# Optimization experiments

Hardware: AMD Instinct MI355X
Metric: run time of the kernel (lower is better)

The kernel has to match this reference:

```python
import jax, jax.numpy as jnp
import numpy as np

N_NODES = 50000
N_EDGES = 800000
D = 64  # all feature sizes


def setup_inputs() -> dict:
    key = jax.random.key(0)
    ks = jax.random.split(key, 16)

    def unif(k, shape, fan_out):
        stdv = 0.2 / np.sqrt(fan_out)
        return jax.random.uniform(k, shape, jnp.float32, -stdv, stdv)

    return {
        "Skipnode_in_feats": jax.random.normal(ks[0], (N_NODES, D), jnp.float32),
        "node_in_feats": jax.random.normal(ks[1], (N_NODES, D), jnp.float32),
        "edge_in_feats": jax.random.normal(ks[2], (N_EDGES, D), jnp.float32),
        "src": jax.random.randint(ks[3], (N_EDGES,), 0, N_NODES, jnp.int32),
        "dst": jax.random.randint(ks[4], (N_EDGES,), 0, N_NODES, jnp.int32),
        "weight_n2n_u": unif(ks[5], (D, D), D),
        "weight_n2n_v": unif(ks[6], (3 * D, D), D),
        "weight_e2n": unif(ks[7], (D, D), D),
        "bias_n": unif(ks[8], (D,), D),
        "weight_n2e_u": unif(ks[9], (D, D), D),
        "weight_n2e_v": unif(ks[10], (2 * D, D), D),
        "weight_e2e": unif(ks[11], (2 * D, D), D),
        "bias_e": unif(ks[12], (D,), D),
    }


def reference(Skipnode_in_feats, node_in_feats, edge_in_feats, src, dst,
              weight_n2n_u, weight_n2n_v, weight_e2n, bias_n,
              weight_n2e_u, weight_n2e_v, weight_e2e, bias_e):
    n_nodes = node_in_feats.shape[0]

    # node -> node messages: m_e = (X W_u)[src] + (E W_e2n)[e], mean over dst
    h1 = node_in_feats @ weight_n2n_u            # [N, D]
    e1 = edge_in_feats @ weight_e2n              # [E, D]
    m = h1[src] + e1                             # [E, D]
    summed = jax.ops.segment_sum(m, dst, num_segments=n_nodes)          # [N, D]
    deg = jax.ops.segment_sum(jnp.ones_like(dst, jnp.float32), dst,
                              num_segments=n_nodes)                     # [N]
    h_neigh = summed / jnp.maximum(deg, 1.0)[:, None]  # DGL mean: 0 for isolated

    h_total = jnp.concatenate([Skipnode_in_feats, node_in_feats, h_neigh], axis=1)
    h_out = h_total @ weight_n2n_v + bias_n      # [N, D]

    # edge update: e2 = (X W_n2e_u)[src] + ([S,X] W_n2e_v)[dst]
    hu = node_in_feats @ weight_n2e_u            # [N, D]
    hc = jnp.concatenate([Skipnode_in_feats, node_in_feats], axis=1)
    hv = hc @ weight_n2e_v                       # [N, D]
    e2 = hu[src] + hv[dst]                       # [E, D]
    e_total = jnp.concatenate([edge_in_feats, e2], axis=1)
    e_out = e_total @ weight_e2e + bias_e        # [E, D]

    return (h_out, e_out)
```

## Files before the change

### kernel.cpp

```cpp
#include <hip/hip_runtime.h>

#define N_NODES 50000
#define N_EDGES 800000
#define D 64
#define ET_PAD 68
#define NB 196

__global__ void fold_weights(const float* __restrict__ w_n2n_u,
                             const float* __restrict__ w_n2n_v,
                             const float* __restrict__ w_e2n,
                             const float* __restrict__ w_n2e_u,
                             const float* __restrict__ w_n2e_v,
                             float* __restrict__ w_e2e_dummy,
                             const float* __restrict__ w_e2e,
                             float* __restrict__ Wbig, float* __restrict__ WD) {
    int bidx = blockIdx.x;
    int j = threadIdx.x;
    const float* Ebot = w_e2e + 64 * 64;
    const float* Wv3  = w_n2n_v + 128 * 64;
    if (bidx < 512) {
        int k = bidx >> 2, q = bidx & 3;
        float v = 0.f;
        if (q == 0) {
            v = w_n2n_v[k * 64 + j];
        } else if (q == 1) {
            if (k >= 64) for (int t = 0; t < 64; ++t) v = fmaf(w_n2e_u[(k - 64) * 64 + t], Ebot[t * 64 + j], v);
        } else if (q == 2) {
            for (int t = 0; t < 64; ++t) v = fmaf(w_n2e_v[k * 64 + t], Ebot[t * 64 + j], v);
        } else {
            if (k >= 64) for (int t = 0; t < 64; ++t) v = fmaf(w_n2n_u[(k - 64) * 64 + t], Wv3[t * 64 + j], v);
        }
        Wbig[(size_t)k * 256 + q * 64 + j] = v;
    } else {
        int k = bidx - 512;
        float v = 0.f;
        for (int t = 0; t < 64; ++t) v = fmaf(w_e2n[k * 64 + t], Wv3[t * 64 + j], v);
        WD[k * 64 + j] = v;
    }
}

__global__ __launch_bounds__(256) void node_pre(
    const float* __restrict__ S, const float* __restrict__ X,
    const float* __restrict__ Wbig, const float* __restrict__ bias_n,
    float* __restrict__ h_out, float* __restrict__ AX, float* __restrict__ bvec) {
    __shared__ __align__(16) float inT[64 * ET_PAD];
    __shared__ __align__(16) float Wl[64 * 64];
    const int t = threadIdx.x;
    const int m0 = blockIdx.x * 64, q = blockIdx.y, c0 = q * 64;
    const int tx = t & 15, ty = t >> 4;
    float acc[4][4] = {{0.f}};
    for (int h = 0; h < 2; ++h) {
        const float* P = h ? X : S;
        #pragma unroll
        for (int i = 0; i < 16; ++i) {
            int idx = i * 256 + t;
            int ml = idx >> 6, kl = idx & 63;
            int m = m0 + ml;
            inT[kl * ET_PAD + ml] = (m < N_NODES) ? P[(size_t)m * 64 + kl] : 0.f;
        }
        #pragma unroll
        for (int i = 0; i < 16; ++i) {
            int idx = i * 256 + t;
            int kl = idx >> 6, jl = idx & 63;
            Wl[kl * 64 + jl] = Wbig[(size_t)(h * 64 + kl) * 256 + c0 + jl];
        }
        __syncthreads();
        #pragma unroll 4
        for (int kl = 0; kl < 64; ++kl) {
            float4 av = *(const float4*)&inT[kl * ET_PAD + ty * 4];
            float4 wv = *(const float4*)&Wl[kl * 64 + tx * 4];
            float a4[4] = {av.x, av.y, av.z, av.w};
            float w4[4] = {wv.x, wv.y, wv.z, wv.w};
            #pragma unroll
            for (int im = 0; im < 4; ++im)
                #pragma unroll
                for (int ij = 0; ij < 4; ++ij)
                    acc[im][ij] = fmaf(a4[im], w4[ij], acc[im][ij]);
        }
        __syncthreads();
    }
    #pragma unroll
    for (int im = 0; im < 4; ++im) {
        int m = m0 + ty * 4 + im;
        if (m >= N_NODES) continue;
        #pragma unroll
        for (int ij = 0; ij < 4; ++ij) {
            int jl = tx * 4 + ij;
            float v = acc[im][ij];
            if (q == 0)      h_out[(size_t)m * 64 + jl] = v + bias_n[jl];
            else if (q == 1) AX[(size_t)m * 128 + 2 * jl] = v;
            else if (q == 2) bvec[(size_t)m * 64 + jl] = v;
            else             AX[(size_t)m * 128 + 2 * jl + 1] = v;
        }
    }
}

__global__ void hist_k(const int* __restrict__ dst, int* __restrict__ counts) {
    int e = blockIdx.x * 256 + threadIdx.x;
    if (e < N_EDGES) atomicAdd(&counts[dst[e]], 1);
}

__global__ void scan1(const int* __restrict__ counts, int* __restrict__ bsum) {
    __shared__ int s[256];
    int t = threadIdx.x;
    int i = blockIdx.x * 256 + t;
    s[t] = (i < N_NODES) ? counts[i] : 0;
    __syncthreads();
    for (int off = 128; off > 0; off >>= 1) {
        if (t < off) s[t] += s[t + off];
        __syncthreads();
    }
    if (t == 0) bsum[blockIdx.x] = s[0];
}

__global__ void scan2(const int* __restrict__ bsum, int* __restrict__ boff) {
    __shared__ int s[256];
    int t = threadIdx.x;
    int v0 = (t < NB) ? bsum[t] : 0;
    s[t] = v0;
    __syncthreads();
    for (int off = 1; off < 256; off <<= 1) {
        int v = (t >= off) ? s[t - off] : 0;
        __syncthreads();
        s[t] += v;
        __syncthreads();
    }
    if (t < NB) boff[t] = s[t] - v0;
}

__global__ void scan3(const int* __restrict__ counts, const int* __restrict__ boff,
                      int* __restrict__ offsets, int* __restrict__ cursor) {
    __shared__ int s[256];
    int t = threadIdx.x;
    int i = blockIdx.x * 256 + t;
    int v0 = (i < N_NODES) ? counts[i] : 0;
    s[t] = v0;
    __syncthreads();
    for (int off = 1; off < 256; off <<= 1) {
        int v = (t >= off) ? s[t - off] : 0;
        __syncthreads();
        s[t] += v;
        __syncthreads();
    }
    int excl = s[t] - v0 + boff[blockIdx.x];
    if (i < N_NODES) { offsets[i] = excl; cursor[i] = excl; }
    if (i == N_NODES - 1) offsets[N_NODES] = excl + v0;
}

__global__ void scatter_k(const int* __restrict__ src, const int* __restrict__ dst,
                          int* __restrict__ cursor, int* __restrict__ perm,
                          int* __restrict__ sSrc, int* __restrict__ sDst) {
    int e = blockIdx.x * 256 + threadIdx.x;
    if (e < N_EDGES) {
        int d = dst[e];
        int p = atomicAdd(&cursor[d], 1);
        perm[p] = e;
        sSrc[p] = src[e];
        sDst[p] = d;
    }
}

__global__ __launch_bounds__(256) void edge_kernel(
    const float* __restrict__ E, const int* __restrict__ perm,
    const int* __restrict__ sSrc, const int* __restrict__ sDst,
    const float* __restrict__ W1g ,
    const float* __restrict__ WDg,
    const float* __restrict__ AX, const float* __restrict__ bvec,
    const float* __restrict__ bias_e,
    float* __restrict__ e_out, float* __restrict__ hpre) {
    __shared__ int sPerm[64];
    __shared__ int sDstL[64];
    __shared__ __align__(16) float sEt[64 * ET_PAD];

    const int t = threadIdx.x;
    const int p0 = blockIdx.x * 64;
    if (t < 64) {
        sPerm[t] = perm[p0 + t];
        sDstL[t] = sDst[p0 + t];
    }
    __syncthreads();

    const int j = t & 63;
    const int g = t >> 6;

    float acc1[16], acc2[16];
    const float bj = bias_e[j];
    #pragma unroll
    for (int r = 0; r < 16; ++r) {
        int pos = g * 16 + r;
        int is = sSrc[p0 + pos];
        int id = sDstL[pos];
        float2 ax = *(const float2*)&AX[(size_t)is * 128 + 2 * j];
        acc1[r] = bj + ax.x + bvec[(size_t)id * 64 + j];
        acc2[r] = ax.y;
    }

    #pragma unroll
    for (int i = 0; i < 16; ++i) {
        int idx = i * 256 + t;
        int r = idx >> 6, k = idx & 63;
        sEt[k * ET_PAD + r] = E[(size_t)sPerm[r] * 64 + k];
    }
    __syncthreads();

    #pragma unroll 4
    for (int k = 0; k < 64; ++k) {
        float w1 = W1g[k * 64 + j];
        float wd = WDg[k * 64 + j];
        const float4* ep = (const float4*)&sEt[k * ET_PAD + g * 16];
        #pragma unroll
        for (int q = 0; q < 4; ++q) {
            float4 ev = ep[q];
            acc1[4 * q + 0] = fmaf(ev.x, w1, acc1[4 * q + 0]);
            acc2[4 * q + 0] = fmaf(ev.x, wd, acc2[4 * q + 0]);
            acc1[4 * q + 1] = fmaf(ev.y, w1, acc1[4 * q + 1]);
            acc2[4 * q + 1] = fmaf(ev.y, wd, acc2[4 * q + 1]);
            acc1[4 * q + 2] = fmaf(ev.z, w1, acc1[4 * q + 2]);
            acc2[4 * q + 2] = fmaf(ev.z, wd, acc2[4 * q + 2]);
            acc1[4 * q + 3] = fmaf(ev.w, w1, acc1[4 * q + 3]);
            acc2[4 * q + 3] = fmaf(ev.w, wd, acc2[4 * q + 3]);
        }
    }

    #pragma unroll
    for (int r = 0; r < 16; ++r) {
        int e = sPerm[g * 16 + r];
        e_out[(size_t)e * 64 + j] = acc1[r];
    }

    int cur = sDstL[g * 16];
    float run = acc2[0];
    #pragma unroll
    for (int r = 1; r < 16; ++r) {
        int d = sDstL[g * 16 + r];
        if (d == cur) {
            run += acc2[r];
        } else {
            atomicAdd(&hpre[(size_t)cur * 64 + j], run);
            cur = d;
            run = acc2[r];
        }
    }
    atomicAdd(&hpre[(size_t)cur * 64 + j], run);
}

__global__ void node_final(float* __restrict__ h_out,
                           const float* __restrict__ hpre,
                           const int* __restrict__ offsets) {
    int i = blockIdx.x * blockDim.x + threadIdx.x;
    if (i < N_NODES * 64) {
        int n = i >> 6;
        float deg = (float)(offsets[n + 1] - offsets[n]);
        float r = 1.0f / fmaxf(deg, 1.0f);
        h_out[i] += hpre[i] * r;
    }
}

extern "C" void kernel_launch(void* const* d_in, const int* in_sizes, int n_in,
                              void* d_out, int out_size, void* d_ws, size_t ws_size,
                              hipStream_t stream) {
    const float* S       = (const float*)d_in[0];
    const float* X       = (const float*)d_in[1];
    const float* E       = (const float*)d_in[2];
    const int*   src     = (const int*)  d_in[3];
    const int*   dst     = (const int*)  d_in[4];
    const float* w_n2n_u = (const float*)d_in[5];
    const float* w_n2n_v = (const float*)d_in[6];
    const float* w_e2n   = (const float*)d_in[7];
    const float* bias_n  = (const float*)d_in[8];
    const float* w_n2e_u = (const float*)d_in[9];
    const float* w_n2e_v = (const float*)d_in[10];
    const float* w_e2e   = (const float*)d_in[11];
    const float* bias_e  = (const float*)d_in[12];

    const size_t ND = (size_t)N_NODES * 64;

    float* ws        = (float*)d_ws;
    float* hpre      = ws;
    int*   counts    = (int*)(ws + ND);
    int*   offsets   = counts + N_NODES;
    int*   cursor    = offsets + N_NODES + 1;
    int*   bsum      = cursor + N_NODES;
    int*   boff      = bsum + 200;
    int*   perm      = boff + 200;
    int*   sSrc      = perm + N_EDGES;
    int*   sDst      = sSrc + N_EDGES;
    float* AX        = (float*)(sDst + N_EDGES);
    float* bvec      = AX + (size_t)N_NODES * 128;
    float* Wbig      = bvec + ND;
    float* WD        = Wbig + 128 * 256;

    float* h_out = (float*)d_out;
    float* e_out = h_out + ND;

    hipMemsetAsync(hpre, 0, (ND + N_NODES) * sizeof(float), stream);

    fold_weights<<<576, 64, 0, stream>>>(w_n2n_u, w_n2n_v, w_e2n, w_n2e_u,
                                         w_n2e_v, nullptr, w_e2e, Wbig, WD);

    dim3 npGrid((N_NODES + 63) / 64, 4);
    node_pre<<<npGrid, 256, 0, stream>>>(S, X, Wbig, bias_n, h_out, AX, bvec);

    hist_k <<<(N_EDGES + 255) / 256, 256, 0, stream>>>(dst, counts);
    scan1  <<<NB, 256, 0, stream>>>(counts, bsum);
    scan2  <<<1, 256, 0, stream>>>(bsum, boff);
    scan3  <<<NB, 256, 0, stream>>>(counts, boff, offsets, cursor);
    scatter_k<<<(N_EDGES + 255) / 256, 256, 0, stream>>>(src, dst, cursor, perm, sSrc, sDst);

    edge_kernel<<<N_EDGES / 64, 256, 0, stream>>>(
        E, perm, sSrc, sDst, w_e2e, WD, AX, bvec, bias_e, e_out, hpre);

    node_final<<<(N_NODES * 64 + 255) / 256, 256, 0, stream>>>(h_out, hpre, offsets);
}
```

Measured before the change: 743.7 us.

## Use bf16 MFMA for edge GEMM and pack sorted edge records

Moves the per-edge 64x128 projection from scalar FMAs on an fp32 LDS tile to bf16 MFMA 16x16x32. Edge features and the concatenated weight matrix (w_e2e top plus folded WD) are converted to bf16. The scatter now writes packed int4 records (perm, src, dst) instead of three separate arrays, and each wave handles its own 16 edges without block-wide syncs. The goal is to cut ALU time and index-load traffic, at the cost of bf16 rounding error on the E-dependent terms.

```diff
diff --git a/kernel.cpp b/kernel.cpp
--- a/kernel.cpp
+++ b/kernel.cpp
@@ -6,14 +6,23 @@
 #define ET_PAD 68
 #define NB 196
 
+typedef __attribute__((ext_vector_type(8))) short short8;
+typedef __attribute__((ext_vector_type(4))) float f32x4;
+
+__device__ inline unsigned short f2bf(float f) {
+    unsigned u = __float_as_uint(f);
+    unsigned r = (u + 0x7FFFu + ((u >> 16) & 1u)) >> 16;
+    return (unsigned short)r;
+}
+
 __global__ void fold_weights(const float* __restrict__ w_n2n_u,
                              const float* __restrict__ w_n2n_v,
                              const float* __restrict__ w_e2n,
                              const float* __restrict__ w_n2e_u,
                              const float* __restrict__ w_n2e_v,
-                             float* __restrict__ w_e2e_dummy,
                              const float* __restrict__ w_e2e,
-                             float* __restrict__ Wbig, float* __restrict__ WD) {
+                             float* __restrict__ Wbig,
+                             unsigned short* __restrict__ WTbf) {
     int bidx = blockIdx.x;
     int j = threadIdx.x;
     const float* Ebot = w_e2e + 64 * 64;
@@ -31,11 +40,14 @@
             if (k >= 64) for (int t = 0; t < 64; ++t) v = fmaf(w_n2n_u[(k - 64) * 64 + t], Wv3[t * 64 + j], v);
         }
         Wbig[(size_t)k * 256 + q * 64 + j] = v;
-    } else {
+    } else if (bidx < 576) {
         int k = bidx - 512;
         float v = 0.f;
         for (int t = 0; t < 64; ++t) v = fmaf(w_e2n[k * 64 + t], Wv3[t * 64 + j], v);
-        WD[k * 64 + j] = v;
+        WTbf[(64 + j) * 64 + k] = f2bf(v);
+    } else {
+        int k = bidx - 576;
+        WTbf[j * 64 + k] = f2bf(w_e2e[k * 64 + j]);
     }
 }
 
@@ -148,96 +160,89 @@
 }
 
 __global__ void scatter_k(const int* __restrict__ src, const int* __restrict__ dst,
-                          int* __restrict__ cursor, int* __restrict__ perm,
-                          int* __restrict__ sSrc, int* __restrict__ sDst) {
+                          int* __restrict__ cursor, int4* __restrict__ sEdge) {
     int e = blockIdx.x * 256 + threadIdx.x;
     if (e < N_EDGES) {
         int d = dst[e];
         int p = atomicAdd(&cursor[d], 1);
-        perm[p] = e;
-        sSrc[p] = src[e];
-        sDst[p] = d;
+        sEdge[p] = make_int4(e, src[e], d, 0);
     }
 }
 
 __global__ __launch_bounds__(256) void edge_kernel(
-    const float* __restrict__ E, const int* __restrict__ perm,
-    const int* __restrict__ sSrc, const int* __restrict__ sDst,
-    const float* __restrict__ W1g ,
-    const float* __restrict__ WDg,
+    const float* __restrict__ E, const int4* __restrict__ sEdge,
+    const unsigned short* __restrict__ WTbf,
     const float* __restrict__ AX, const float* __restrict__ bvec,
     const float* __restrict__ bias_e,
     float* __restrict__ e_out, float* __restrict__ hpre) {
-    __shared__ int sPerm[64];
-    __shared__ int sDstL[64];
-    __shared__ __align__(16) float sEt[64 * ET_PAD];
+    __shared__ __align__(16) unsigned short sEt[64 * 64];
+    __shared__ __align__(16) float sOut[64 * 128];
 
     const int t = threadIdx.x;
+    const int lane = t & 63;
+    const int w = t >> 6;
     const int p0 = blockIdx.x * 64;
-    if (t < 64) {
-        sPerm[t] = perm[p0 + t];
-        sDstL[t] = sDst[p0 + t];
-    }
-    __syncthreads();
-
-    const int j = t & 63;
-    const int g = t >> 6;
-
-    float acc1[16], acc2[16];
+    const int l15 = lane & 15, qd = lane >> 4;
+    const int j = lane;
+
+    float2 axv[16];
+    float  bv[16];
+    int    permv[16], dstv[16];
+    #pragma unroll
+    for (int r = 0; r < 16; ++r) {
+        int4 ed = sEdge[p0 + 16 * w + r];
+        permv[r] = ed.x;
+        dstv[r]  = ed.z;
+        axv[r] = *(const float2*)&AX[(size_t)ed.y * 128 + 2 * j];
+        bv[r]  = bvec[(size_t)ed.z * 64 + j];
+    }
+
+    #pragma unroll
+    for (int i = 0; i < 8; ++i) {
+        int idx = i * 64 + lane;
+        int r  = idx >> 5;
+        int kp = idx & 31;
+        int pe = sEdge[p0 + 16 * w + r].x;
+        float2 ev = *(const float2*)&E[(size_t)pe * 64 + 2 * kp];
+        unsigned pk = ((unsigned)f2bf(ev.y) << 16) | (unsigned)f2bf(ev.x);
+        *(unsigned*)&sEt[(16 * w + r) * 64 + 2 * kp] = pk;
+    }
+
+    const short8 a0 = *(const short8*)&sEt[(16 * w + l15) * 64 +  0 + qd * 8];
+    const short8 a1 = *(const short8*)&sEt[(16 * w + l15) * 64 + 32 + qd * 8];
+    #pragma unroll
+    for (int tt = 0; tt < 8; ++tt) {
+        const short8 b0 = *(const short8*)&WTbf[(16 * tt + l15) * 64 +  0 + qd * 8];
+        const short8 b1 = *(const short8*)&WTbf[(16 * tt + l15) * 64 + 32 + qd * 8];
+        f32x4 d = {0.f, 0.f, 0.f, 0.f};
+        d = __builtin_amdgcn_mfma_f32_16x16x32_bf16(a0, b0, d, 0, 0, 0);
+        d = __builtin_amdgcn_mfma_f32_16x16x32_bf16(a1, b1, d, 0, 0, 0);
+        int colw = (tt < 4) ? (16 * tt + l15) : (16 * (tt - 4) + l15);
+        int pos  = (tt < 4) ? (2 * colw) : (2 * colw + 1);
+        #pragma unroll
+        for (int reg = 0; reg < 4; ++reg)
+            sOut[(16 * w + qd * 4 + reg) * 128 + pos] = d[reg];
+    }
+
     const float bj = bias_e[j];
+    float acc2[16];
     #pragma unroll
     for (int r = 0; r < 16; ++r) {
-        int pos = g * 16 + r;
-        int is = sSrc[p0 + pos];
-        int id = sDstL[pos];
-        float2 ax = *(const float2*)&AX[(size_t)is * 128 + 2 * j];
-        acc1[r] = bj + ax.x + bvec[(size_t)id * 64 + j];
-        acc2[r] = ax.y;
-    }
-
-    #pragma unroll
-    for (int i = 0; i < 16; ++i) {
-        int idx = i * 256 + t;
-        int r = idx >> 6, k = idx & 63;
-        sEt[k * ET_PAD + r] = E[(size_t)sPerm[r] * 64 + k];
-    }
-    __syncthreads();
-
-    #pragma unroll 4
-    for (int k = 0; k < 64; ++k) {
-        float w1 = W1g[k * 64 + j];
-        float wd = WDg[k * 64 + j];
-        const float4* ep = (const float4*)&sEt[k * ET_PAD + g * 16];
-        #pragma unroll
-        for (int q = 0; q < 4; ++q) {
-            float4 ev = ep[q];
-            acc1[4 * q + 0] = fmaf(ev.x, w1, acc1[4 * q + 0]);
-            acc2[4 * q + 0] = fmaf(ev.x, wd, acc2[4 * q + 0]);
-            acc1[4 * q + 1] = fmaf(ev.y, w1, acc1[4 * q + 1]);
-            acc2[4 * q + 1] = fmaf(ev.y, wd, acc2[4 * q + 1]);
-            acc1[4 * q + 2] = fmaf(ev.z, w1, acc1[4 * q + 2]);
-            acc2[4 * q + 2] = fmaf(ev.z, wd, acc2[4 * q + 2]);
-            acc1[4 * q + 3] = fmaf(ev.w, w1, acc1[4 * q + 3]);
-            acc2[4 * q + 3] = fmaf(ev.w, wd, acc2[4 * q + 3]);
-        }
-    }
-
-    #pragma unroll
-    for (int r = 0; r < 16; ++r) {
-        int e = sPerm[g * 16 + r];
-        e_out[(size_t)e * 64 + j] = acc1[r];
-    }
-
-    int cur = sDstL[g * 16];
+        float2 o = *(const float2*)&sOut[(16 * w + r) * 128 + 2 * j];
+        float v1 = o.x + bj + axv[r].x + bv[r];
+        acc2[r]  = o.y + axv[r].y;
+        e_out[(size_t)permv[r] * 64 + j] = v1;
+    }
+
+    int cur = dstv[0];
     float run = acc2[0];
     #pragma unroll
     for (int r = 1; r < 16; ++r) {
-        int d = sDstL[g * 16 + r];
-        if (d == cur) {
+        if (dstv[r] == cur) {
             run += acc2[r];
         } else {
             atomicAdd(&hpre[(size_t)cur * 64 + j], run);
-            cur = d;
+            cur = dstv[r];
             run = acc2[r];
         }
     }
@@ -275,28 +280,27 @@
 
     const size_t ND = (size_t)N_NODES * 64;
 
-    float* ws        = (float*)d_ws;
-    float* hpre      = ws;
-    int*   counts    = (int*)(ws + ND);
-    int*   offsets   = counts + N_NODES;
-    int*   cursor    = offsets + N_NODES + 1;
-    int*   bsum      = cursor + N_NODES;
-    int*   boff      = bsum + 200;
-    int*   perm      = boff + 200;
-    int*   sSrc      = perm + N_EDGES;
-    int*   sDst      = sSrc + N_EDGES;
-    float* AX        = (float*)(sDst + N_EDGES);
-    float* bvec      = AX + (size_t)N_NODES * 128;
-    float* Wbig      = bvec + ND;
-    float* WD        = Wbig + 128 * 256;
+    float* ws = (float*)d_ws;
+    float*          hpre    = ws;
+    float*          AX      = ws + ND;
+    float*          bvec    = AX + (size_t)N_NODES * 128;
+    float*          Wbig    = bvec + ND;
+    unsigned short* WTbf    = (unsigned short*)(Wbig + 128 * 256);
+    int*            counts  = (int*)(WTbf + 8192);
+    int4*           sEdge   = (int4*)(counts + N_NODES);
+    int*            offsets = (int*)(sEdge + N_EDGES);
+    int*            cursor  = offsets + N_NODES + 1;
+    int*            bsum    = cursor + N_NODES;
+    int*            boff    = bsum + 200;
 
     float* h_out = (float*)d_out;
     float* e_out = h_out + ND;
 
-    hipMemsetAsync(hpre, 0, (ND + N_NODES) * sizeof(float), stream);
-
-    fold_weights<<<576, 64, 0, stream>>>(w_n2n_u, w_n2n_v, w_e2n, w_n2e_u,
-                                         w_n2e_v, nullptr, w_e2e, Wbig, WD);
+    hipMemsetAsync(hpre, 0, ND * sizeof(float), stream);
+    hipMemsetAsync(counts, 0, N_NODES * sizeof(int), stream);
+
+    fold_weights<<<640, 64, 0, stream>>>(w_n2n_u, w_n2n_v, w_e2n, w_n2e_u,
+                                         w_n2e_v, w_e2e, Wbig, WTbf);
 
     dim3 npGrid((N_NODES + 63) / 64, 4);
     node_pre<<<npGrid, 256, 0, stream>>>(S, X, Wbig, bias_n, h_out, AX, bvec);
@@ -305,10 +309,10 @@
     scan1  <<<NB, 256, 0, stream>>>(counts, bsum);
     scan2  <<<1, 256, 0, stream>>>(bsum, boff);
     scan3  <<<NB, 256, 0, stream>>>(counts, boff, offsets, cursor);
-    scatter_k<<<(N_EDGES + 255) / 256, 256, 0, stream>>>(src, dst, cursor, perm, sSrc, sDst);
+    scatter_k<<<(N_EDGES + 255) / 256, 256, 0, stream>>>(src, dst, cursor, sEdge);
 
     edge_kernel<<<N_EDGES / 64, 256, 0, stream>>>(
-        E, perm, sSrc, sDst, w_e2e, WD, AX, bvec, bias_e, e_out, hpre);
+        E, sEdge, WTbf, AX, bvec, bias_e, e_out, hpre);
 
     node_final<<<(N_NODES * 64 + 255) / 256, 256, 0, stream>>>(h_out, hpre, offsets);
 }
```

After: 725.1 us. -2.5%, faster.
